# Kernel optimization log

Measured on AMD Instinct MI355X. Metric: run time of the kernel, lower is better.

## Reference

```python
import jax, jax.numpy as jnp
from jax import lax
import numpy as np

B = 65536
DIM_OBS = 9
DIM_ACT = 4
H = 192
DN = ('NCHW', 'OIHW', 'NCHW')


def _conv(x, w, stride):
    return lax.conv_general_dilated(x, w, (stride, stride), 'VALID', dimension_numbers=DN)


def setup_inputs() -> dict:
    key = jax.random.key(0)
    ks = jax.random.split(key, 16)
    n = lambda k, shp, s: (jax.random.normal(k, shp, dtype=jnp.float32) * s)
    inp = {
        'x': n(ks[0], (B, 1, 12, 16), 1.0),
        'v': n(ks[1], (B, DIM_OBS), 1.0),
        'hx': n(ks[2], (B, H), 1.0),
        # stem convs (no bias)
        'w1': n(ks[3], (32, 1, 2, 2), 0.5),
        'w2': n(ks[4], (64, 32, 3, 3), 0.06),
        'w3': n(ks[5], (128, 64, 3, 3), 0.04),
        'w_stem': n(ks[6], (H, 128 * 2 * 4), 0.03),   # Linear(1024, 192, bias=False)
        # v_proj (weight scaled by 0.5 as in __init__)
        'w_vproj': n(ks[7], (H, DIM_OBS), 0.5 / np.sqrt(DIM_OBS)),
        'b_vproj': n(ks[8], (H,), 0.1),
        # GRUCell(192, 192): gate order r, z, n
        'w_ih': n(ks[9], (3 * H, H), 1.0 / np.sqrt(H)),
        'w_hh': n(ks[10], (3 * H, H), 1.0 / np.sqrt(H)),
        'b_ih': n(ks[11], (3 * H,), 0.05),
        'b_hh': n(ks[12], (3 * H,), 0.05),
        # fc (weight scaled by 0.01 as in __init__)
        'w_fc': n(ks[13], (DIM_ACT, H), 0.01 / np.sqrt(H)),
    }
    return inp


def reference(x, v, hx, w1, w2, w3, w_stem, w_vproj, b_vproj,
              w_ih, w_hh, b_ih, b_hh, w_fc):
    lrelu = lambda t: jax.nn.leaky_relu(t, 0.05)
    # vision stem: [B,1,12,16] -> [B,32,6,8] -> [B,64,4,6] -> [B,128,2,4]
    h = lrelu(_conv(x, w1, 2))
    h = lrelu(_conv(h, w2, 1))
    h = lrelu(_conv(h, w3, 1))
    img_feat = h.reshape(h.shape[0], -1) @ w_stem.T          # [B,192]
    state_feat = v @ w_vproj.T + b_vproj                      # [B,192]
    fused = lrelu(img_feat + state_feat)
    # GRUCell (torch gate order: r, z, n)
    gi = fused @ w_ih.T + b_ih                                # [B,576]
    gh = hx @ w_hh.T + b_hh                                   # [B,576]
    ir, iz, i_n = jnp.split(gi, 3, axis=-1)
    hr, hz, h_n = jnp.split(gh, 3, axis=-1)
    r = jax.nn.sigmoid(ir + hr)
    z = jax.nn.sigmoid(iz + hz)
    n = jnp.tanh(i_n + r * h_n)
    hx_new = (1.0 - z) * n + z * hx
    act = lrelu(hx_new) @ w_fc.T                              # [B,4]
    return act, hx_new
```

## Files before the change

### kernel.cpp

```cpp
#include <hip/hip_runtime.h>


typedef short bf8 __attribute__((ext_vector_type(8)));
typedef float f4  __attribute__((ext_vector_type(4)));

#define MFMA(a, b, c) __builtin_amdgcn_mfma_f32_16x16x32_bf16(a, b, c, 0, 0, 0)

#define W3_OFF    18432
#define WSTEM_OFF 92160
#define WIH_OFF   294912
#define WHH_OFF   405504
#define W_TOTAL   516096
#define C3_OFF    (1 << 20)
#define C2Q_OFF   68157440

__device__ __forceinline__ unsigned short f2bf(float f) {
    unsigned int u = __float_as_uint(f);
    u += 0x7fffu + ((u >> 16) & 1u);
    return (unsigned short)(u >> 16);
}
__device__ __forceinline__ float bf2f(unsigned short h) {
    return __uint_as_float(((unsigned int)h) << 16);
}
__device__ __forceinline__ float lrelu(float v) { return v > 0.f ? v : 0.05f * v; }
__device__ __forceinline__ float sigm(float x) { return 1.f / (1.f + __expf(-x)); }
__device__ __forceinline__ float tanh_(float x) {
    float e = __expf(2.f * x);
    return 1.f - 2.f / (e + 1.f);
}

__global__ void prep_weights(const float* __restrict__ w2, const float* __restrict__ w3,
                             const float* __restrict__ wstem, const float* __restrict__ wvp,
                             const float* __restrict__ wih, const float* __restrict__ whh,
                             unsigned short* __restrict__ o) {
    int i = blockIdx.x * 256 + threadIdx.x;
    if (i >= W_TOTAL) return;
    float val;
    if (i < W3_OFF) {
        int n = i / 288, k = i - n * 288;
        val = w2[n * 288 + (k & 31) * 9 + (k >> 5)];
    } else if (i < WSTEM_OFF) {
        int d = i - W3_OFF;
        int n = d / 576, k = d - n * 576;
        val = w3[n * 576 + (k & 63) * 9 + (k >> 6)];
    } else if (i < WIH_OFF) {
        int d = i - WSTEM_OFF;
        int n = d / 1056, k = d - n * 1056;
        if (k < 1024)       val = wstem[(n << 10) + (k & 127) * 8 + (k >> 7)];
        else if (k < 1033)  val = wvp[n * 9 + (k - 1024)];
        else                val = 0.f;
    } else if (i < WHH_OFF) {
        val = wih[i - WIH_OFF];
    } else {
        val = whh[i - WHH_OFF];
    }
    o[i] = f2bf(val);
}

__global__ __launch_bounds__(256, 2) void conv12(
    const float* __restrict__ x, const float* __restrict__ w1,
    const unsigned short* __restrict__ ws, unsigned short* __restrict__ c2q,
    int sbase)
{
    __shared__ __align__(16) unsigned short lds[6144];
    const int tid = threadIdx.x;
    const int wave = tid >> 6, lane = tid & 63;
    const int col = lane & 15, quad = lane >> 4;
    const int W0 = blockIdx.x * 16;

    bf8 Bf2[9];
    int kq2[9];
    #pragma unroll
    for (int ks = 0; ks < 9; ++ks) {
        int k0 = ks * 32 + quad * 8;
        Bf2[ks] = *(const bf8*)(ws + (wave * 16 + col) * 288 + k0);
        int ky = k0 / 96, r = k0 - 96 * ky;
        kq2[ks] = (ky * 8 + (r >> 5)) * 32 + (r & 31);
    }
    const int g = wave * 2 + (col >> 3);

    for (int c = 0; c < 4; ++c) {
        if (tid < 192) {
            int s = tid / 48, p = tid - s * 48;
            int y = p >> 3, xx = p & 7;
            const float* xp = x + (size_t)(sbase + W0 + c * 4 + s) * 192 + y * 32 + xx * 2;
            float x00 = xp[0], x01 = xp[1], x10 = xp[16], x11 = xp[17];
            int base = s * 1536, sw = (s & 3) << 3;
            #pragma unroll
            for (int cc = 0; cc < 32; ++cc) {
                int co = (cc + p) & 31;
                float a = x00 * w1[co * 4] + x01 * w1[co * 4 + 1]
                        + x10 * w1[co * 4 + 2] + x11 * w1[co * 4 + 3];
                lds[base + ((p * 32 + co) ^ sw)] = f2bf(lrelu(a));
            }
        }
        __syncthreads();

        #pragma unroll
        for (int mt2 = 0; mt2 < 3; ++mt2) {
            int m0 = mt2 * 32 + col, m1 = m0 + 16;
            int s0 = m0 & 3, p0 = m0 >> 2;
            int s1 = m1 & 3, p1 = m1 >> 2;
            int oy0 = p0 / 6, ox0 = p0 - 6 * oy0;
            int oy1 = p1 / 6, ox1 = p1 - 6 * oy1;
            int b0 = s0 * 1536, qb0 = (oy0 * 8 + ox0) * 32, sw0 = (s0 & 3) << 3;
            int b1 = s1 * 1536, qb1 = (oy1 * 8 + ox1) * 32, sw1 = (s1 & 3) << 3;
            f4 acc0 = {0.f, 0.f, 0.f, 0.f}, acc1 = {0.f, 0.f, 0.f, 0.f};
            #pragma unroll
            for (int ks = 0; ks < 9; ++ks) {
                bf8 a0 = *(const bf8*)&lds[b0 + ((qb0 + kq2[ks]) ^ sw0)];
                bf8 a1 = *(const bf8*)&lds[b1 + ((qb1 + kq2[ks]) ^ sw1)];
                acc0 = MFMA(a0, Bf2[ks], acc0);
                acc1 = MFMA(a1, Bf2[ks], acc1);
            }
            #pragma unroll
            for (int r = 0; r < 4; ++r) {
                int m = mt2 * 32 + quad * 4 + r;
                int s = m & 3, pos = m >> 2;
                int sloc = W0 + c * 4 + s;
                int key = (pos + ((sloc & 1) << 2)) & 7;
                c2q[(size_t)sloc * 1536 + pos * 64 + ((g ^ key) << 3) + (col & 7)]
                    = f2bf(lrelu(acc0[r]));
                m += 16; s = m & 3; pos = m >> 2;
                sloc = W0 + c * 4 + s;
                key = (pos + ((sloc & 1) << 2)) & 7;
                c2q[(size_t)sloc * 1536 + pos * 64 + ((g ^ key) << 3) + (col & 7)]
                    = f2bf(lrelu(acc1[r]));
            }
        }
        __syncthreads();
    }
}

__global__ __launch_bounds__(256, 2) void conv3k(
    const unsigned short* __restrict__ ws, const unsigned short* __restrict__ c2q,
    unsigned short* __restrict__ c3, int sbase)
{
    __shared__ __align__(16) unsigned short lds[12288];
    const int tid = threadIdx.x;
    const int wave = tid >> 6, lane = tid & 63;
    const int col = lane & 15, quad = lane >> 4;
    const int h = blockIdx.x & 1;
    const int Q0 = (blockIdx.x >> 1) * 32;
    const int n_in = h * 64 + wave * 16 + col;

    bf8 Bf3[18];
    #pragma unroll
    for (int ks = 0; ks < 18; ++ks)
        Bf3[ks] = *(const bf8*)(ws + W3_OFF + n_in * 576 + ks * 32 + quad * 8);

    int aoff[18];
    {
        int opos = col & 7;
        int oy = opos >> 2, ox = opos & 3;
        int spar = (col >> 3) & 1;
        #pragma unroll
        for (int ks = 0; ks < 18; ++ks) {
            int k0 = ks * 32 + quad * 8;
            int b = k0 >> 6;
            int ky = b / 3, kx = b - 3 * ky;
            int pos2 = (oy + ky) * 6 + (ox + kx);
            int gg = (k0 & 63) >> 3;
            int key = (pos2 + (spar << 2)) & 7;
            aoff[ks] = pos2 * 64 + ((gg ^ key) << 3);
        }
    }
    const int Gl = h * 8 + wave * 2 + (col >> 3);

    for (int c = 0; c < 4; ++c) {
        const unsigned short* s2 = c2q + (size_t)(Q0 + c * 8) * 1536 + tid * 48;
        #pragma unroll
        for (int i = 0; i < 6; ++i)
            *(bf8*)&lds[tid * 48 + i * 8] = *(const bf8*)(s2 + i * 8);
        __syncthreads();

        f4 acc[4];
        #pragma unroll
        for (int mt = 0; mt < 4; ++mt) acc[mt] = (f4){0.f, 0.f, 0.f, 0.f};
        #pragma unroll
        for (int ks = 0; ks < 18; ++ks) {
            #pragma unroll
            for (int mt = 0; mt < 4; ++mt) {
                int sc = mt * 2 + (col >> 3);
                bf8 a = *(const bf8*)&lds[sc * 1536 + aoff[ks]];
                acc[mt] = MFMA(a, Bf3[ks], acc[mt]);
            }
        }
        #pragma unroll
        for (int mt = 0; mt < 4; ++mt) {
            #pragma unroll
            for (int r = 0; r < 4; ++r) {
                int m = quad * 4 + r;
                int sc = mt * 2 + (m >> 3), opos = m & 7;
                int srow = sbase + Q0 + c * 8 + sc;
                c3[(size_t)srow * 1024 + opos * 128 + ((Gl ^ (srow & 15)) << 3) + (col & 7)]
                    = f2bf(lrelu(acc[mt][r]));
            }
        }
        __syncthreads();
    }
}

__global__ __launch_bounds__(256, 2) void stem_gru(
    const unsigned short* __restrict__ ws, const float* __restrict__ v,
    const float* __restrict__ hx, const float* __restrict__ bvp,
    const float* __restrict__ bih, const float* __restrict__ bhh,
    const float* __restrict__ wfc, float* __restrict__ out)
{
    __shared__ __align__(16) unsigned short lds[24576];
    const int tid = threadIdx.x;
    const int wave = tid >> 6, lane = tid & 63;
    const int col = lane & 15, quad = lane >> 4;
    const int S0 = blockIdx.x * 64;
    const unsigned short* c3 = ws + C3_OFF;
    const unsigned short* wstem = ws + WSTEM_OFF;

    f4 acc[4][3];
    #pragma unroll
    for (int mt = 0; mt < 4; ++mt)
        #pragma unroll
        for (int t = 0; t < 3; ++t) acc[mt][t] = (f4){0.f, 0.f, 0.f, 0.f};

    const int sm = tid >> 2, sq = tid & 3;
    const unsigned short* asrc = c3 + (size_t)(S0 + sm) * 1024 + sq * 32;

    #pragma unroll
    for (int i = 0; i < 4; ++i)
        *(bf8*)&lds[12288 + sm * 128 + sq * 32 + i * 8] = *(const bf8*)(asrc + i * 8);

    for (int kc = 0; kc < 8; ++kc) {
        __syncthreads();
        bf8 nx[4];
        if (kc < 7) {
            const unsigned short* s2 = asrc + (kc + 1) * 128;
            #pragma unroll
            for (int i = 0; i < 4; ++i) nx[i] = *(const bf8*)(s2 + i * 8);
        }
        #pragma unroll
        for (int ks = 0; ks < 4; ++ks) {
            int kl = ks * 32 + quad * 8;
            int kk = kc * 128 + kl;
            bf8 b0 = *(const bf8*)(wstem + (wave * 48 + col) * 1056 + kk);
            bf8 b1 = *(const bf8*)(wstem + (wave * 48 + 16 + col) * 1056 + kk);
            bf8 b2 = *(const bf8*)(wstem + (wave * 48 + 32 + col) * 1056 + kk);
            #pragma unroll
            for (int mt = 0; mt < 4; ++mt) {
                int m = mt * 16 + col;
                bf8 a = *(const bf8*)&lds[12288 + m * 128 + (kl ^ ((m & 15) << 3))];
                acc[mt][0] = MFMA(a, b0, acc[mt][0]);
                acc[mt][1] = MFMA(a, b1, acc[mt][1]);
                acc[mt][2] = MFMA(a, b2, acc[mt][2]);
            }
        }
        __syncthreads();
        if (kc < 7) {
            #pragma unroll
            for (int i = 0; i < 4; ++i)
                *(bf8*)&lds[12288 + sm * 128 + sq * 32 + i * 8] = nx[i];
        }
    }

    if (tid < 64) {
        int m = tid;
        const float* vp = v + (size_t)(S0 + m) * 9;
        __align__(16) unsigned short tmp[32];
        #pragma unroll
        for (int i = 0; i < 9; ++i) tmp[i] = f2bf(vp[i]);
        #pragma unroll
        for (int i = 9; i < 32; ++i) tmp[i] = 0;
        #pragma unroll
        for (int gg = 0; gg < 4; ++gg) {
            int gp = gg ^ (m & 15);
            *(bf8*)&lds[12288 + m * 128 + gp * 8] = *(bf8*)&tmp[gg * 8];
        }
    }
    __syncthreads();
    {
        int kl = quad * 8;
        bf8 b0 = *(const bf8*)(wstem + (wave * 48 + col) * 1056 + 1024 + kl);
        bf8 b1 = *(const bf8*)(wstem + (wave * 48 + 16 + col) * 1056 + 1024 + kl);
        bf8 b2 = *(const bf8*)(wstem + (wave * 48 + 32 + col) * 1056 + 1024 + kl);
        #pragma unroll
        for (int mt = 0; mt < 4; ++mt) {
            int m = mt * 16 + col;
            bf8 a = *(const bf8*)&lds[12288 + m * 128 + (kl ^ ((m & 15) << 3))];
            acc[mt][0] = MFMA(a, b0, acc[mt][0]);
            acc[mt][1] = MFMA(a, b1, acc[mt][1]);
            acc[mt][2] = MFMA(a, b2, acc[mt][2]);
        }
    }

    #pragma unroll
    for (int t = 0; t < 3; ++t) {
        int n = wave * 48 + t * 16 + col;
        float bb = bvp[n];
        #pragma unroll
        for (int mt = 0; mt < 4; ++mt)
            #pragma unroll
            for (int r = 0; r < 4; ++r) {
                int m = mt * 16 + quad * 4 + r;
                lds[m * 192 + (n ^ ((m & 7) << 3))] = f2bf(lrelu(acc[mt][t][r] + bb));
            }
    }
    __syncthreads();

    {
        int m = tid >> 2, qq = tid & 3;
        const float* hp = hx + (size_t)(S0 + m) * 192 + qq * 48;
        #pragma unroll
        for (int i = 0; i < 6; ++i) {
            f4 d = *(const f4*)(hp + i * 8 + 0);
            f4 d2 = *(const f4*)(hp + i * 8 + 4);
            __align__(16) unsigned short tmp[8];
            #pragma unroll
            for (int u = 0; u < 4; ++u) { tmp[u] = f2bf(d[u]); tmp[4 + u] = f2bf(d2[u]); }
            int gg = qq * 6 + i, gp = gg ^ (m & 7);
            *(bf8*)&lds[12288 + m * 192 + gp * 8] = *(bf8*)tmp;
        }
    }
    __syncthreads();

    #pragma unroll
    for (int t = 0; t < 3; ++t) {
        int j0 = (wave * 3 + t) * 16;
        int j = j0 + col;
        const unsigned short* pih = ws + WIH_OFF + j * 192;
        const unsigned short* phh = ws + WHH_OFF + j * 192;
        f4 g0[4], g1[4], g2[4], g3[4], g4[4], g5[4];
        #pragma unroll
        for (int mt = 0; mt < 4; ++mt) {
            g0[mt] = (f4){0.f,0.f,0.f,0.f}; g1[mt] = g0[mt]; g2[mt] = g0[mt];
            g3[mt] = g0[mt]; g4[mt] = g0[mt]; g5[mt] = g0[mt];
        }
        #pragma unroll
        for (int ks = 0; ks < 6; ++ks) {
            int k0 = ks * 32 + quad * 8;
            bf8 bir = *(const bf8*)(pih + k0);
            bf8 bhr = *(const bf8*)(phh + k0);
            bf8 biz = *(const bf8*)(pih + 36864 + k0);
            bf8 bhz = *(const bf8*)(phh + 36864 + k0);
            bf8 bin = *(const bf8*)(pih + 73728 + k0);
            bf8 bhn = *(const bf8*)(phh + 73728 + k0);
            #pragma unroll
            for (int mt = 0; mt < 4; ++mt) {
                int m = mt * 16 + col;
                int off = m * 192 + (k0 ^ ((m & 7) << 3));
                bf8 aF = *(const bf8*)&lds[off];
                bf8 aH = *(const bf8*)&lds[12288 + off];
                g0[mt] = MFMA(aF, bir, g0[mt]);
                g1[mt] = MFMA(aH, bhr, g1[mt]);
                g2[mt] = MFMA(aF, biz, g2[mt]);
                g3[mt] = MFMA(aH, bhz, g3[mt]);
                g4[mt] = MFMA(aF, bin, g4[mt]);
                g5[mt] = MFMA(aH, bhn, g5[mt]);
            }
        }
        float b_ir = bih[j], b_iz = bih[192 + j], b_in = bih[384 + j];
        float b_hr = bhh[j], b_hz = bhh[192 + j], b_hn = bhh[384 + j];
        #pragma unroll
        for (int mt = 0; mt < 4; ++mt)
            #pragma unroll
            for (int r = 0; r < 4; ++r) {
                int s = mt * 16 + quad * 4 + r;
                float rg = sigm(g0[mt][r] + b_ir + g1[mt][r] + b_hr);
                float zg = sigm(g2[mt][r] + b_iz + g3[mt][r] + b_hz);
                float ng = tanh_(g4[mt][r] + b_in + rg * (g5[mt][r] + b_hn));
                float hxv = hx[(size_t)(S0 + s) * 192 + j];
                float hnew = (1.f - zg) * ng + zg * hxv;
                out[65536 * 4 + (size_t)(S0 + s) * 192 + j] = hnew;
            }
    }
    __syncthreads();

    {
        int s = tid & 63, a = tid >> 6;
        const float* hp = out + 65536 * 4 + (size_t)(S0 + s) * 192;
        const float* wf = wfc + a * 192;
        float sum = 0.f;
        #pragma unroll 4
        for (int jj = 0; jj < 48; ++jj) {
            f4 hv = *(const f4*)(hp + jj * 4);
            f4 wv = *(const f4*)(wf + jj * 4);
            #pragma unroll
            for (int u = 0; u < 4; ++u) sum += lrelu(hv[u]) * wv[u];
        }
        out[(size_t)(S0 + s) * 4 + a] = sum;
    }
}

extern "C" void kernel_launch(void* const* d_in, const int* in_sizes, int n_in,
                              void* d_out, int out_size, void* d_ws, size_t ws_size,
                              hipStream_t stream) {
    const float* x     = (const float*)d_in[0];
    const float* v     = (const float*)d_in[1];
    const float* hx    = (const float*)d_in[2];
    const float* w1    = (const float*)d_in[3];
    const float* w2    = (const float*)d_in[4];
    const float* w3    = (const float*)d_in[5];
    const float* wstem = (const float*)d_in[6];
    const float* wvp   = (const float*)d_in[7];
    const float* bvp   = (const float*)d_in[8];
    const float* wih   = (const float*)d_in[9];
    const float* whh   = (const float*)d_in[10];
    const float* bih   = (const float*)d_in[11];
    const float* bhh   = (const float*)d_in[12];
    const float* wfc   = (const float*)d_in[13];
    unsigned short* wsp = (unsigned short*)d_ws;
    unsigned short* c3  = wsp + C3_OFF;
    unsigned short* c2q = wsp + C2Q_OFF;

    prep_weights<<<2016, 256, 0, stream>>>(w2, w3, wstem, wvp, wih, whh, wsp);
    for (int q = 0; q < 4; ++q) {
        conv12<<<1024, 256, 0, stream>>>(x, w1, wsp, c2q, q * 16384);
        conv3k<<<1024, 256, 0, stream>>>(wsp, c2q, c3, q * 16384);
    }
    stem_gru<<<1024, 256, 0, stream>>>(wsp, v, hx, bvp, bih, bhh, wfc, (float*)d_out);
}
```

Measured before the change: 587.0 us.

## Fuse conv1/conv2 and conv3 kernels, keeping conv2 output in LDS

Merges the conv12 and conv3k kernels into one 512-thread kernel. Conv2 output now goes into shared memory and is read by conv3 directly, so it no longer makes a round trip through a global scratch buffer. This also removes the eight per-quarter launches. In exchange, only half the waves do conv2 work, occupancy drops to one block per CU, and each block holds 48KB of LDS.

```diff
diff --git a/kernel.cpp b/kernel.cpp
--- a/kernel.cpp
+++ b/kernel.cpp
@@ -12,7 +12,6 @@
 #define WHH_OFF   405504
 #define W_TOTAL   516096
 #define C3_OFF    (1 << 20)
-#define C2Q_OFF   68157440
 
 __device__ __forceinline__ unsigned short f2bf(float f) {
     unsigned int u = __float_as_uint(f);
@@ -57,93 +56,31 @@
     o[i] = f2bf(val);
 }
 
-__global__ __launch_bounds__(256, 2) void conv12(
+__global__ __launch_bounds__(512, 1) void convfused(
     const float* __restrict__ x, const float* __restrict__ w1,
-    const unsigned short* __restrict__ ws, unsigned short* __restrict__ c2q,
-    int sbase)
+    const unsigned short* __restrict__ ws, unsigned short* __restrict__ c3)
 {
-    __shared__ __align__(16) unsigned short lds[6144];
+    __shared__ __align__(16) unsigned short lds[24576];
     const int tid = threadIdx.x;
     const int wave = tid >> 6, lane = tid & 63;
     const int col = lane & 15, quad = lane >> 4;
-    const int W0 = blockIdx.x * 16;
+    const int W0 = blockIdx.x * 64;
+    const int w4 = wave & 3, h = wave >> 2;
 
     bf8 Bf2[9];
     int kq2[9];
-    #pragma unroll
-    for (int ks = 0; ks < 9; ++ks) {
-        int k0 = ks * 32 + quad * 8;
-        Bf2[ks] = *(const bf8*)(ws + (wave * 16 + col) * 288 + k0);
-        int ky = k0 / 96, r = k0 - 96 * ky;
-        kq2[ks] = (ky * 8 + (r >> 5)) * 32 + (r & 31);
-    }
-    const int g = wave * 2 + (col >> 3);
-
-    for (int c = 0; c < 4; ++c) {
-        if (tid < 192) {
-            int s = tid / 48, p = tid - s * 48;
-            int y = p >> 3, xx = p & 7;
-            const float* xp = x + (size_t)(sbase + W0 + c * 4 + s) * 192 + y * 32 + xx * 2;
-            float x00 = xp[0], x01 = xp[1], x10 = xp[16], x11 = xp[17];
-            int base = s * 1536, sw = (s & 3) << 3;
-            #pragma unroll
-            for (int cc = 0; cc < 32; ++cc) {
-                int co = (cc + p) & 31;
-                float a = x00 * w1[co * 4] + x01 * w1[co * 4 + 1]
-                        + x10 * w1[co * 4 + 2] + x11 * w1[co * 4 + 3];
-                lds[base + ((p * 32 + co) ^ sw)] = f2bf(lrelu(a));
-            }
-        }
-        __syncthreads();
-
-        #pragma unroll
-        for (int mt2 = 0; mt2 < 3; ++mt2) {
-            int m0 = mt2 * 32 + col, m1 = m0 + 16;
-            int s0 = m0 & 3, p0 = m0 >> 2;
-            int s1 = m1 & 3, p1 = m1 >> 2;
-            int oy0 = p0 / 6, ox0 = p0 - 6 * oy0;
-            int oy1 = p1 / 6, ox1 = p1 - 6 * oy1;
-            int b0 = s0 * 1536, qb0 = (oy0 * 8 + ox0) * 32, sw0 = (s0 & 3) << 3;
-            int b1 = s1 * 1536, qb1 = (oy1 * 8 + ox1) * 32, sw1 = (s1 & 3) << 3;
-            f4 acc0 = {0.f, 0.f, 0.f, 0.f}, acc1 = {0.f, 0.f, 0.f, 0.f};
-            #pragma unroll
-            for (int ks = 0; ks < 9; ++ks) {
-                bf8 a0 = *(const bf8*)&lds[b0 + ((qb0 + kq2[ks]) ^ sw0)];
-                bf8 a1 = *(const bf8*)&lds[b1 + ((qb1 + kq2[ks]) ^ sw1)];
-                acc0 = MFMA(a0, Bf2[ks], acc0);
-                acc1 = MFMA(a1, Bf2[ks], acc1);
-            }
-            #pragma unroll
-            for (int r = 0; r < 4; ++r) {
-                int m = mt2 * 32 + quad * 4 + r;
-                int s = m & 3, pos = m >> 2;
-                int sloc = W0 + c * 4 + s;
-                int key = (pos + ((sloc & 1) << 2)) & 7;
-                c2q[(size_t)sloc * 1536 + pos * 64 + ((g ^ key) << 3) + (col & 7)]
-                    = f2bf(lrelu(acc0[r]));
-                m += 16; s = m & 3; pos = m >> 2;
-                sloc = W0 + c * 4 + s;
-                key = (pos + ((sloc & 1) << 2)) & 7;
-                c2q[(size_t)sloc * 1536 + pos * 64 + ((g ^ key) << 3) + (col & 7)]
-                    = f2bf(lrelu(acc1[r]));
-            }
-        }
-        __syncthreads();
-    }
-}
-
-__global__ __launch_bounds__(256, 2) void conv3k(
-    const unsigned short* __restrict__ ws, const unsigned short* __restrict__ c2q,
-    unsigned short* __restrict__ c3, int sbase)
-{
-    __shared__ __align__(16) unsigned short lds[12288];
-    const int tid = threadIdx.x;
-    const int wave = tid >> 6, lane = tid & 63;
-    const int col = lane & 15, quad = lane >> 4;
-    const int h = blockIdx.x & 1;
-    const int Q0 = (blockIdx.x >> 1) * 32;
-    const int n_in = h * 64 + wave * 16 + col;
-
+    if (wave < 4) {
+        #pragma unroll
+        for (int ks = 0; ks < 9; ++ks) {
+            int k0 = ks * 32 + quad * 8;
+            Bf2[ks] = *(const bf8*)(ws + (wave * 16 + col) * 288 + k0);
+            int ky = k0 / 96, r = k0 - 96 * ky;
+            kq2[ks] = (ky * 8 + (r >> 5)) * 32 + (r & 31);
+        }
+    }
+    const int g = w4 * 2 + (col >> 3);
+
+    const int n_in = h * 64 + w4 * 16 + col;
     bf8 Bf3[18];
     #pragma unroll
     for (int ks = 0; ks < 18; ++ks)
@@ -165,36 +102,91 @@
             aoff[ks] = pos2 * 64 + ((gg ^ key) << 3);
         }
     }
-    const int Gl = h * 8 + wave * 2 + (col >> 3);
-
-    for (int c = 0; c < 4; ++c) {
-        const unsigned short* s2 = c2q + (size_t)(Q0 + c * 8) * 1536 + tid * 48;
-        #pragma unroll
-        for (int i = 0; i < 6; ++i)
-            *(bf8*)&lds[tid * 48 + i * 8] = *(const bf8*)(s2 + i * 8);
+    const int Gl = h * 8 + w4 * 2 + (col >> 3);
+
+    for (int c8 = 0; c8 < 8; ++c8) {
+        if (tid < 192) {
+            int sl0 = tid / 48, p = tid - sl0 * 48;
+            int y = p >> 3, xx = p & 7;
+            #pragma unroll
+            for (int ss = 0; ss < 2; ++ss) {
+                int sl = sl0 + ss * 4;
+                const float* xp = x + (size_t)(W0 + c8 * 8 + sl) * 192 + y * 32 + xx * 2;
+                float x00 = xp[0], x01 = xp[1], x10 = xp[16], x11 = xp[17];
+                int base = sl * 1536, sw = (sl & 3) << 3;
+                #pragma unroll
+                for (int cc = 0; cc < 32; ++cc) {
+                    int co = (cc + p) & 31;
+                    float a = x00 * w1[co * 4] + x01 * w1[co * 4 + 1]
+                            + x10 * w1[co * 4 + 2] + x11 * w1[co * 4 + 3];
+                    lds[base + ((p * 32 + co) ^ sw)] = f2bf(lrelu(a));
+                }
+            }
+        }
         __syncthreads();
 
-        f4 acc[4];
-        #pragma unroll
-        for (int mt = 0; mt < 4; ++mt) acc[mt] = (f4){0.f, 0.f, 0.f, 0.f};
-        #pragma unroll
-        for (int ks = 0; ks < 18; ++ks) {
+        if (wave < 4) {
+            #pragma unroll
+            for (int sub = 0; sub < 2; ++sub) {
+                #pragma unroll
+                for (int mt2 = 0; mt2 < 3; ++mt2) {
+                    int m0 = mt2 * 32 + col, m1 = m0 + 16;
+                    int s0 = m0 & 3, p0 = m0 >> 2;
+                    int s1 = m1 & 3, p1 = m1 >> 2;
+                    int oy0 = p0 / 6, ox0 = p0 - 6 * oy0;
+                    int oy1 = p1 / 6, ox1 = p1 - 6 * oy1;
+                    int b0 = (sub * 4 + s0) * 1536, qb0 = (oy0 * 8 + ox0) * 32, sw0 = (s0 & 3) << 3;
+                    int b1 = (sub * 4 + s1) * 1536, qb1 = (oy1 * 8 + ox1) * 32, sw1 = (s1 & 3) << 3;
+                    f4 acc0 = {0.f, 0.f, 0.f, 0.f}, acc1 = {0.f, 0.f, 0.f, 0.f};
+                    #pragma unroll
+                    for (int ks = 0; ks < 9; ++ks) {
+                        bf8 a0 = *(const bf8*)&lds[b0 + ((qb0 + kq2[ks]) ^ sw0)];
+                        bf8 a1 = *(const bf8*)&lds[b1 + ((qb1 + kq2[ks]) ^ sw1)];
+                        acc0 = MFMA(a0, Bf2[ks], acc0);
+                        acc1 = MFMA(a1, Bf2[ks], acc1);
+                    }
+                    #pragma unroll
+                    for (int r = 0; r < 4; ++r) {
+                        int m = mt2 * 32 + quad * 4 + r;
+                        int s = m & 3, pos = m >> 2;
+                        int slc = sub * 4 + s;
+                        int key = (pos + ((slc & 1) << 2)) & 7;
+                        lds[12288 + slc * 1536 + pos * 64 + ((g ^ key) << 3) + (col & 7)]
+                            = f2bf(lrelu(acc0[r]));
+                        m += 16; s = m & 3; pos = m >> 2;
+                        slc = sub * 4 + s;
+                        key = (pos + ((slc & 1) << 2)) & 7;
+                        lds[12288 + slc * 1536 + pos * 64 + ((g ^ key) << 3) + (col & 7)]
+                            = f2bf(lrelu(acc1[r]));
+                    }
+                }
+            }
+        }
+        __syncthreads();
+
+        {
+            f4 acc[4];
+            #pragma unroll
+            for (int mt = 0; mt < 4; ++mt) acc[mt] = (f4){0.f, 0.f, 0.f, 0.f};
+            #pragma unroll
+            for (int ks = 0; ks < 18; ++ks) {
+                #pragma unroll
+                for (int mt = 0; mt < 4; ++mt) {
+                    int sc = mt * 2 + (col >> 3);
+                    bf8 a = *(const bf8*)&lds[12288 + sc * 1536 + aoff[ks]];
+                    acc[mt] = MFMA(a, Bf3[ks], acc[mt]);
+                }
+            }
             #pragma unroll
             for (int mt = 0; mt < 4; ++mt) {
-                int sc = mt * 2 + (col >> 3);
-                bf8 a = *(const bf8*)&lds[sc * 1536 + aoff[ks]];
-                acc[mt] = MFMA(a, Bf3[ks], acc[mt]);
-            }
-        }
-        #pragma unroll
-        for (int mt = 0; mt < 4; ++mt) {
-            #pragma unroll
-            for (int r = 0; r < 4; ++r) {
-                int m = quad * 4 + r;
-                int sc = mt * 2 + (m >> 3), opos = m & 7;
-                int srow = sbase + Q0 + c * 8 + sc;
-                c3[(size_t)srow * 1024 + opos * 128 + ((Gl ^ (srow & 15)) << 3) + (col & 7)]
-                    = f2bf(lrelu(acc[mt][r]));
+                #pragma unroll
+                for (int r = 0; r < 4; ++r) {
+                    int m = quad * 4 + r;
+                    int sc = mt * 2 + (m >> 3), opos = m & 7;
+                    int srow = W0 + c8 * 8 + sc;
+                    c3[(size_t)srow * 1024 + opos * 128 + ((Gl ^ (srow & 15)) << 3) + (col & 7)]
+                        = f2bf(lrelu(acc[mt][r]));
+                }
             }
         }
         __syncthreads();
@@ -407,12 +399,8 @@
     const float* wfc   = (const float*)d_in[13];
     unsigned short* wsp = (unsigned short*)d_ws;
     unsigned short* c3  = wsp + C3_OFF;
-    unsigned short* c2q = wsp + C2Q_OFF;
 
     prep_weights<<<2016, 256, 0, stream>>>(w2, w3, wstem, wvp, wih, whh, wsp);
-    for (int q = 0; q < 4; ++q) {
-        conv12<<<1024, 256, 0, stream>>>(x, w1, wsp, c2q, q * 16384);
-        conv3k<<<1024, 256, 0, stream>>>(wsp, c2q, c3, q * 16384);
-    }
+    convfused<<<1024, 512, 0, stream>>>(x, w1, wsp, c3);
     stem_gru<<<1024, 256, 0, stream>>>(wsp, v, hx, bvp, bih, bhh, wfc, (float*)d_out);
 }
```

Measured after the change: 1.279 ms. 2.18x slower.
